# Kernel optimization log

Hardware: AMD Instinct MI355X
Metric: run time of the kernel (lower is better)

Reference implementation:

```python
import jax, jax.numpy as jnp
import numpy as np

B, T, D, E, C = 4, 4096, 2048, 8, 1024
H = D // E  # per-expert hidden = out_features // num_experts = 256


def setup_inputs() -> dict:
    key = jax.random.key(0)
    ks = jax.random.split(key, 7)
    x = jax.random.normal(ks[0], (B, T, D), dtype=jnp.float32)
    # nn.Linear-style init scale ~ 1/sqrt(fan_in)
    W1 = jax.random.normal(ks[1], (E, H, D), dtype=jnp.float32) / np.sqrt(D)
    b1 = jax.random.normal(ks[2], (E, H), dtype=jnp.float32) / np.sqrt(D)
    W2 = jax.random.normal(ks[3], (E, D, H), dtype=jnp.float32) / np.sqrt(D)
    b2 = jax.random.normal(ks[4], (D,), dtype=jnp.float32) / np.sqrt(D)
    expert_indices = jax.random.randint(ks[5], (B, E, C), 0, T, dtype=jnp.int32)
    expert_gate = jax.random.uniform(ks[6], (B, E, C), dtype=jnp.float32)
    return {"x": x, "W1": W1, "b1": b1, "W2": W2, "b2": b2,
            "expert_indices": expert_indices, "expert_gate": expert_gate,
            "num_tokens": T}


def reference(x, W1, b1, W2, b2, expert_indices, expert_gate, num_tokens):
    # x: (B,T,D); expert_indices/expert_gate: (B,E,C)
    Bb = x.shape[0]
    Ee, Cc = expert_indices.shape[1], expert_indices.shape[2]
    b_idx = jnp.arange(Bb)[:, None, None]
    # dispatch: gather tokens per expert -> (B,E,C,D)
    sel = x[b_idx, expert_indices]
    # contract: per-expert GEMM -> (B,E,C,H)
    h = jnp.einsum('becd,ehd->bech', sel, W1) + b1[None, :, None, :]
    h = jax.nn.gelu(h, approximate=False)
    # expand: per-expert GEMM -> (B,E,C,D), shared output bias
    y = jnp.einsum('bech,eoh->beco', h, W2) + b2
    y = y * expert_gate[..., None]
    # combine: gated scatter-add back to token positions -> (B,T,D)
    out = jnp.zeros((Bb, num_tokens, x.shape[2]), dtype=x.dtype)
    out = out.at[jnp.arange(Bb)[:, None], expert_indices.reshape(Bb, Ee * Cc)].add(
        y.reshape(Bb, Ee * Cc, -1))
    return out
```

## Files before the change

kernel.cpp:

```cpp
#include <hip/hip_runtime.h>
#include <math.h>

#define B_ 4
#define T_ 4096
#define D_ 2048
#define E_ 8
#define C_ 1024
#define H_ 256
#define SLOTCAP 32

typedef unsigned short u16;
typedef unsigned long long u64;
typedef __attribute__((ext_vector_type(8))) short short8;
typedef __attribute__((ext_vector_type(4))) float f32x4;

__device__ __forceinline__ u16 f2bf(float f) {
    union { float f; unsigned u; } v; v.f = f;
    unsigned r = (v.u + 0x7FFFu + ((v.u >> 16) & 1u)) >> 16;
    return (u16)r;
}
__device__ __forceinline__ float bf2f(u16 u) {
    union { unsigned u; float f; } v; v.u = ((unsigned)u) << 16;
    return v.f;
}

__device__ __forceinline__ int swz(int row, int chunk) {
    return (row << 6) + ((chunk ^ (row & 7)) << 3);
}

__global__ __launch_bounds__(256) void conv_f32_bf16(
    const float* __restrict__ src, u16* __restrict__ dst, int n)
{
    int i = (blockIdx.x * 256 + threadIdx.x) * 4;
    if (i >= n) return;
    f32x4 v = *reinterpret_cast<const f32x4*>(src + i);
    u16 o[4];
    o[0] = f2bf(v[0]); o[1] = f2bf(v[1]); o[2] = f2bf(v[2]); o[3] = f2bf(v[3]);
    *reinterpret_cast<u64*>(dst + i) = *reinterpret_cast<const u64*>(o);
}

__global__ __launch_bounds__(512) void gemm1_v3(
    const float* __restrict__ x, const u16* __restrict__ W1bf,
    const float* __restrict__ b1, const int* __restrict__ idx,
    u16* __restrict__ Hbuf)
{
    const int mt = blockIdx.x;
    const int be = blockIdx.y;
    const int b = be >> 3, e = be & 7;
    const int m0 = mt * 128;

    __shared__ __align__(16) u16 As[2][128 * 64];
    __shared__ __align__(16) u16 Bs[2][256 * 64];
    __shared__ int toks[128];
    __shared__ float bs1[256];

    const int tid = threadIdx.x;
    if (tid < 128) toks[tid] = idx[(b * E_ + e) * C_ + m0 + tid];
    if (tid < 256) bs1[tid] = b1[e * H_ + tid];
    __syncthreads();

    const int lane = tid & 63, wid = tid >> 6;
    const int wm = wid >> 2, wn = wid & 3;
    const int l15 = lane & 15, lk = lane >> 4;

    const int ar = tid >> 2, ac0 = tid & 3;
    const float* aRow = x + (size_t)b * (T_ * (size_t)D_)
                          + (size_t)toks[ar] * D_;
    const int br = tid >> 1, bc0 = (tid & 1) * 4;
    const u16* bRow = W1bf + ((size_t)e * H_ + br) * D_;

    const int aOff0 = swz(ar, ac0), aOff1 = swz(ar, ac0 + 4);
    int bOff[4];
    #pragma unroll
    for (int j = 0; j < 4; ++j) bOff[j] = swz(br, bc0 + j);

    f32x4 acc[4][4];
    #pragma unroll
    for (int i = 0; i < 4; ++i)
        #pragma unroll
        for (int j = 0; j < 4; ++j)
            acc[i][j] = (f32x4){0.f, 0.f, 0.f, 0.f};

    f32x4 pa[4];
    short8 pb[4];

#define G1_LOAD(k)                                                            \
    do {                                                                      \
        pa[0] = *reinterpret_cast<const f32x4*>(aRow + (k) + ac0 * 8);        \
        pa[1] = *reinterpret_cast<const f32x4*>(aRow + (k) + ac0 * 8 + 4);    \
        pa[2] = *reinterpret_cast<const f32x4*>(aRow + (k) + (ac0 + 4) * 8);  \
        pa[3] = *reinterpret_cast<const f32x4*>(aRow + (k) + (ac0 + 4) * 8 + 4);\
        _Pragma("unroll")                                                     \
        for (int j = 0; j < 4; ++j)                                           \
            pb[j] = *reinterpret_cast<const short8*>(bRow + (k) + (bc0 + j) * 8);\
    } while (0)

#define G1_WRITE(buf)                                                         \
    do {                                                                      \
        short8 s0, s1;                                                        \
        _Pragma("unroll")                                                     \
        for (int r = 0; r < 4; ++r) {                                         \
            s0[r] = (short)f2bf(pa[0][r]); s0[r + 4] = (short)f2bf(pa[1][r]); \
            s1[r] = (short)f2bf(pa[2][r]); s1[r + 4] = (short)f2bf(pa[3][r]); \
        }                                                                     \
        *reinterpret_cast<short8*>(&As[buf][aOff0]) = s0;                     \
        *reinterpret_cast<short8*>(&As[buf][aOff1]) = s1;                     \
        _Pragma("unroll")                                                     \
        for (int j = 0; j < 4; ++j)                                           \
            *reinterpret_cast<short8*>(&Bs[buf][bOff[j]]) = pb[j];            \
    } while (0)

    G1_LOAD(0);
    G1_WRITE(0);
    G1_LOAD(64);
    asm volatile("s_waitcnt lgkmcnt(0)" ::: "memory");
    __builtin_amdgcn_s_barrier();

    const int NT = D_ / 64;
    for (int t = 0; t < NT; ++t) {
        const int cur = t & 1;
        if (t + 1 < NT) G1_WRITE(cur ^ 1);
        if (t + 2 < NT) G1_LOAD((t + 2) * 64);
        #pragma unroll
        for (int kk = 0; kk < 2; ++kk) {
            short8 af[4], bfr[4];
            #pragma unroll
            for (int m = 0; m < 4; ++m) {
                const int row = wm * 64 + m * 16 + l15;
                af[m] = *reinterpret_cast<const short8*>(
                    &As[cur][swz(row, kk * 4 + lk)]);
            }
            #pragma unroll
            for (int n = 0; n < 4; ++n) {
                const int row = wn * 64 + n * 16 + l15;
                bfr[n] = *reinterpret_cast<const short8*>(
                    &Bs[cur][swz(row, kk * 4 + lk)]);
            }
            #pragma unroll
            for (int m = 0; m < 4; ++m)
                #pragma unroll
                for (int n = 0; n < 4; ++n)
                    acc[m][n] = __builtin_amdgcn_mfma_f32_16x16x32_bf16(
                        bfr[n], af[m], acc[m][n], 0, 0, 0);
        }
        asm volatile("s_waitcnt lgkmcnt(0)" ::: "memory");
        __builtin_amdgcn_s_barrier();
    }
#undef G1_LOAD
#undef G1_WRITE

    const size_t hbase = ((size_t)(b * E_ + e) * C_ + m0) * H_;
    #pragma unroll
    for (int m = 0; m < 4; ++m) {
        const int cl = wm * 64 + m * 16 + l15;
        u16* rowp = Hbuf + hbase + (size_t)cl * H_;
        #pragma unroll
        for (int n = 0; n < 4; ++n) {
            const int hb = wn * 64 + n * 16 + lk * 4;
            u16 o[4];
            #pragma unroll
            for (int r = 0; r < 4; ++r) {
                float h = acc[m][n][r] + bs1[hb + r];
                float g = 0.5f * h * (1.0f + erff(h * 0.70710678118f));
                o[r] = f2bf(g);
            }
            *reinterpret_cast<u64*>(rowp + hb) = *reinterpret_cast<const u64*>(o);
        }
    }
}

__global__ __launch_bounds__(512) void gemm2_v2(
    const u16* __restrict__ Hbuf, const u16* __restrict__ W2bf,
    const float* __restrict__ b2, const float* __restrict__ gate,
    u16* __restrict__ Ybuf)
{
    const int mt = blockIdx.x >> 3, nt = blockIdx.x & 7;
    const int be = blockIdx.y;
    const int b = be >> 3, e = be & 7;
    const int m0 = mt * 128, n0 = nt * 256;

    __shared__ __align__(16) u16 As[128 * 64];
    __shared__ __align__(16) u16 Bs[256 * 64];
    __shared__ float gs[128];
    __shared__ float bs2[256];

    const int tid = threadIdx.x;
    if (tid < 128) gs[tid] = gate[(b * E_ + e) * C_ + m0 + tid];
    if (tid < 256) bs2[tid] = b2[n0 + tid];
    __syncthreads();

    const int lane = tid & 63, wid = tid >> 6;
    const int wm = wid >> 2, wn = wid & 3;
    const int l15 = lane & 15, lk = lane >> 4;

    const int ar = tid >> 2, ac0 = tid & 3;
    const u16* aRow = Hbuf + ((size_t)(b * E_ + e) * C_ + m0 + ar) * H_;
    const int br = tid >> 1, bc0 = (tid & 1) * 4;
    const u16* bRow = W2bf + ((size_t)e * D_ + n0 + br) * H_;

    const int aOff0 = swz(ar, ac0), aOff1 = swz(ar, ac0 + 4);
    int bOff[4];
    #pragma unroll
    for (int j = 0; j < 4; ++j) bOff[j] = swz(br, bc0 + j);

    f32x4 acc[4][4];
    #pragma unroll
    for (int i = 0; i < 4; ++i)
        #pragma unroll
        for (int j = 0; j < 4; ++j)
            acc[i][j] = (f32x4){0.f, 0.f, 0.f, 0.f};

    short8 pa0, pa1, pb[4];
    pa0 = *reinterpret_cast<const short8*>(aRow + ac0 * 8);
    pa1 = *reinterpret_cast<const short8*>(aRow + (ac0 + 4) * 8);
    #pragma unroll
    for (int j = 0; j < 4; ++j)
        pb[j] = *reinterpret_cast<const short8*>(bRow + (bc0 + j) * 8);
    *reinterpret_cast<short8*>(&As[aOff0]) = pa0;
    *reinterpret_cast<short8*>(&As[aOff1]) = pa1;
    #pragma unroll
    for (int j = 0; j < 4; ++j)
        *reinterpret_cast<short8*>(&Bs[bOff[j]]) = pb[j];
    __syncthreads();

    const int NT = H_ / 64;
    for (int t = 0; t < NT; ++t) {
        if (t + 1 < NT) {
            const int k = (t + 1) * 64;
            pa0 = *reinterpret_cast<const short8*>(aRow + k + ac0 * 8);
            pa1 = *reinterpret_cast<const short8*>(aRow + k + (ac0 + 4) * 8);
            #pragma unroll
            for (int j = 0; j < 4; ++j)
                pb[j] = *reinterpret_cast<const short8*>(bRow + k + (bc0 + j) * 8);
        }
        #pragma unroll
        for (int kk = 0; kk < 2; ++kk) {
            short8 af[4], bfr[4];
            #pragma unroll
            for (int m = 0; m < 4; ++m) {
                const int row = wm * 64 + m * 16 + l15;
                af[m] = *reinterpret_cast<const short8*>(&As[swz(row, kk * 4 + lk)]);
            }
            #pragma unroll
            for (int n = 0; n < 4; ++n) {
                const int row = wn * 64 + n * 16 + l15;
                bfr[n] = *reinterpret_cast<const short8*>(&Bs[swz(row, kk * 4 + lk)]);
            }
            #pragma unroll
            for (int m = 0; m < 4; ++m)
                #pragma unroll
                for (int n = 0; n < 4; ++n)
                    acc[m][n] = __builtin_amdgcn_mfma_f32_16x16x32_bf16(
                        bfr[n], af[m], acc[m][n], 0, 0, 0);
        }
        if (t + 1 < NT) {
            __syncthreads();
            *reinterpret_cast<short8*>(&As[aOff0]) = pa0;
            *reinterpret_cast<short8*>(&As[aOff1]) = pa1;
            #pragma unroll
            for (int j = 0; j < 4; ++j)
                *reinterpret_cast<short8*>(&Bs[bOff[j]]) = pb[j];
            __syncthreads();
        }
    }

    const size_t ybase = (size_t)(b * E_ + e) * C_ + m0;
    #pragma unroll
    for (int m = 0; m < 4; ++m) {
        const int cl = wm * 64 + m * 16 + l15;
        const float g = gs[cl];
        u16* rowp = Ybuf + (ybase + cl) * (size_t)D_ + n0;
        #pragma unroll
        for (int n = 0; n < 4; ++n) {
            const int db = wn * 64 + n * 16 + lk * 4;
            u16 o[4];
            #pragma unroll
            for (int r = 0; r < 4; ++r)
                o[r] = f2bf((acc[m][n][r] + bs2[db + r]) * g);
            *reinterpret_cast<u64*>(rowp + db) = *reinterpret_cast<const u64*>(o);
        }
    }
}

__global__ __launch_bounds__(256) void fill_kernel(
    const int* __restrict__ idx, int* __restrict__ cnt,
    int* __restrict__ slots)
{
    int i = blockIdx.x * 256 + threadIdx.x;
    if (i >= B_ * E_ * C_) return;
    int b = i / (E_ * C_);
    int slot = i % (E_ * C_);
    int t = idx[i];
    int p = atomicAdd(&cnt[b * T_ + t], 1);
    if (p < SLOTCAP) slots[(b * T_ + t) * SLOTCAP + p] = slot;
}

__global__ __launch_bounds__(256) void combine_kernel(
    const u16* __restrict__ Ybuf, const int* __restrict__ cnt,
    const int* __restrict__ slots, float* __restrict__ out)
{
    const int bt = blockIdx.x;
    const int tid = threadIdx.x;
    __shared__ int sl[SLOTCAP];
    int n = cnt[bt];
    n = n > SLOTCAP ? SLOTCAP : n;
    if (tid < n) sl[tid] = slots[bt * SLOTCAP + tid];
    __syncthreads();
    const int b = bt >> 12;
    float a[8] = {0.f, 0.f, 0.f, 0.f, 0.f, 0.f, 0.f, 0.f};
    for (int s = 0; s < n; ++s) {
        const u16* yrow = Ybuf + ((size_t)b * (E_ * C_) + sl[s]) * D_ + tid * 8;
        short8 v = *reinterpret_cast<const short8*>(yrow);
        #pragma unroll
        for (int j = 0; j < 8; ++j) a[j] += bf2f((u16)v[j]);
    }
    float* orow = out + (size_t)bt * D_ + tid * 8;
    *reinterpret_cast<f32x4*>(orow)     = (f32x4){a[0], a[1], a[2], a[3]};
    *reinterpret_cast<f32x4*>(orow + 4) = (f32x4){a[4], a[5], a[6], a[7]};
}

extern "C" void kernel_launch(void* const* d_in, const int* in_sizes, int n_in,
                              void* d_out, int out_size, void* d_ws, size_t ws_size,
                              hipStream_t stream) {
    const float* x    = (const float*)d_in[0];
    const float* W1   = (const float*)d_in[1];
    const float* b1   = (const float*)d_in[2];
    const float* W2   = (const float*)d_in[3];
    const float* b2   = (const float*)d_in[4];
    const int*   idx  = (const int*)d_in[5];
    const float* gate = (const float*)d_in[6];
    float* out = (float*)d_out;

    const size_t nW = (size_t)E_ * H_ * D_;
    const size_t nH = (size_t)B_ * E_ * C_ * H_;
    const size_t nY = (size_t)B_ * E_ * C_ * D_;

    u16* W1bf = (u16*)d_ws;
    u16* W2bf = W1bf + nW;
    u16* Hbuf = W2bf + nW;
    u16* Ybuf = Hbuf + nH;
    int* cnt   = (int*)(Ybuf + nY);
    int* slots = cnt + (size_t)B_ * T_;

    hipMemsetAsync(cnt, 0, (size_t)B_ * T_ * sizeof(int), stream);
    conv_f32_bf16<<<(int)(nW / 1024), 256, 0, stream>>>(W1, W1bf, (int)nW);
    conv_f32_bf16<<<(int)(nW / 1024), 256, 0, stream>>>(W2, W2bf, (int)nW);
    fill_kernel<<<(B_ * E_ * C_) / 256, 256, 0, stream>>>(idx, cnt, slots);

    gemm1_v3<<<dim3(8, 32), 512, 0, stream>>>(x, W1bf, b1, idx, Hbuf);
    gemm2_v2<<<dim3(64, 32), 512, 0, stream>>>(Hbuf, W2bf, b2, gate, Ybuf);
    combine_kernel<<<B_ * T_, 256, 0, stream>>>(Ybuf, cnt, slots, out);
}
```

Measured before the change: 219.0 us.

## Split gemm1 into 128x128 tiles with 256-thread blocks and MFMA priority

gemm1 now splits the 256-wide hidden dimension into two 128-column tiles and uses 256-thread blocks with two blocks per CU. This doubles the grid to 512 blocks, which should fill the CUs better and reduce LDS per block. It also raises wave priority around the MFMA loop and switches to the library bf16 conversion. The cost is that each gathered x row is now loaded and converted twice, once per N tile.

```diff
diff --git a/kernel.cpp b/kernel.cpp
--- a/kernel.cpp
+++ b/kernel.cpp
@@ -1,4 +1,5 @@
 #include <hip/hip_runtime.h>
+#include <hip/hip_bf16.h>
 #include <math.h>
 
 #define B_ 4
@@ -19,6 +20,11 @@
     unsigned r = (v.u + 0x7FFFu + ((v.u >> 16) & 1u)) >> 16;
     return (u16)r;
 }
+__device__ __forceinline__ u16 f2bf_n(float f) {
+    union { __hip_bfloat16 b; u16 u; } v;
+    v.b = __float2bfloat16(f);
+    return v.u;
+}
 __device__ __forceinline__ float bf2f(u16 u) {
     union { unsigned u; float f; } v; v.u = ((unsigned)u) << 16;
     return v.f;
@@ -39,40 +45,42 @@
     *reinterpret_cast<u64*>(dst + i) = *reinterpret_cast<const u64*>(o);
 }
 
-__global__ __launch_bounds__(512) void gemm1_v3(
+__global__ __launch_bounds__(256, 2) void gemm1_v4(
     const float* __restrict__ x, const u16* __restrict__ W1bf,
     const float* __restrict__ b1, const int* __restrict__ idx,
     u16* __restrict__ Hbuf)
 {
-    const int mt = blockIdx.x;
+    const int mt = blockIdx.x >> 1, nt = blockIdx.x & 1;
     const int be = blockIdx.y;
     const int b = be >> 3, e = be & 7;
-    const int m0 = mt * 128;
+    const int m0 = mt * 128, n0 = nt * 128;
 
     __shared__ __align__(16) u16 As[2][128 * 64];
-    __shared__ __align__(16) u16 Bs[2][256 * 64];
+    __shared__ __align__(16) u16 Bs[2][128 * 64];
     __shared__ int toks[128];
-    __shared__ float bs1[256];
+    __shared__ float bs1[128];
 
     const int tid = threadIdx.x;
-    if (tid < 128) toks[tid] = idx[(b * E_ + e) * C_ + m0 + tid];
-    if (tid < 256) bs1[tid] = b1[e * H_ + tid];
+    if (tid < 128) {
+        toks[tid] = idx[(b * E_ + e) * C_ + m0 + tid];
+        bs1[tid] = b1[e * H_ + n0 + tid];
+    }
     __syncthreads();
 
     const int lane = tid & 63, wid = tid >> 6;
-    const int wm = wid >> 2, wn = wid & 3;
+    const int wm = wid >> 1, wn = wid & 1;
     const int l15 = lane & 15, lk = lane >> 4;
 
-    const int ar = tid >> 2, ac0 = tid & 3;
+    const int sr = tid >> 1;
+    const int scb = (tid & 1) * 4;
+
     const float* aRow = x + (size_t)b * (T_ * (size_t)D_)
-                          + (size_t)toks[ar] * D_;
-    const int br = tid >> 1, bc0 = (tid & 1) * 4;
-    const u16* bRow = W1bf + ((size_t)e * H_ + br) * D_;
-
-    const int aOff0 = swz(ar, ac0), aOff1 = swz(ar, ac0 + 4);
-    int bOff[4];
-    #pragma unroll
-    for (int j = 0; j < 4; ++j) bOff[j] = swz(br, bc0 + j);
+                          + (size_t)toks[sr] * D_;
+    const u16* bRow = W1bf + ((size_t)e * H_ + n0 + sr) * D_;
+
+    int wOff[4];
+    #pragma unroll
+    for (int j = 0; j < 4; ++j) wOff[j] = swz(sr, scb + j);
 
     f32x4 acc[4][4];
     #pragma unroll
@@ -81,33 +89,32 @@
         for (int j = 0; j < 4; ++j)
             acc[i][j] = (f32x4){0.f, 0.f, 0.f, 0.f};
 
-    f32x4 pa[4];
+    f32x4 pa[8];
     short8 pb[4];
 
-#define G1_LOAD(k)                                                            \
-    do {                                                                      \
-        pa[0] = *reinterpret_cast<const f32x4*>(aRow + (k) + ac0 * 8);        \
-        pa[1] = *reinterpret_cast<const f32x4*>(aRow + (k) + ac0 * 8 + 4);    \
-        pa[2] = *reinterpret_cast<const f32x4*>(aRow + (k) + (ac0 + 4) * 8);  \
-        pa[3] = *reinterpret_cast<const f32x4*>(aRow + (k) + (ac0 + 4) * 8 + 4);\
-        _Pragma("unroll")                                                     \
-        for (int j = 0; j < 4; ++j)                                           \
-            pb[j] = *reinterpret_cast<const short8*>(bRow + (k) + (bc0 + j) * 8);\
+#define G1_LOAD(k)                                                             \
+    do {                                                                       \
+        _Pragma("unroll")                                                      \
+        for (int j = 0; j < 4; ++j) {                                          \
+            pa[2 * j]     = *reinterpret_cast<const f32x4*>(aRow + (k) + (scb + j) * 8);     \
+            pa[2 * j + 1] = *reinterpret_cast<const f32x4*>(aRow + (k) + (scb + j) * 8 + 4); \
+            pb[j] = *reinterpret_cast<const short8*>(bRow + (k) + (scb + j) * 8);            \
+        }                                                                      \
     } while (0)
 
-#define G1_WRITE(buf)                                                         \
-    do {                                                                      \
-        short8 s0, s1;                                                        \
-        _Pragma("unroll")                                                     \
-        for (int r = 0; r < 4; ++r) {                                         \
-            s0[r] = (short)f2bf(pa[0][r]); s0[r + 4] = (short)f2bf(pa[1][r]); \
-            s1[r] = (short)f2bf(pa[2][r]); s1[r + 4] = (short)f2bf(pa[3][r]); \
-        }                                                                     \
-        *reinterpret_cast<short8*>(&As[buf][aOff0]) = s0;                     \
-        *reinterpret_cast<short8*>(&As[buf][aOff1]) = s1;                     \
-        _Pragma("unroll")                                                     \
-        for (int j = 0; j < 4; ++j)                                           \
-            *reinterpret_cast<short8*>(&Bs[buf][bOff[j]]) = pb[j];            \
+#define G1_WRITE(buf)                                                          \
+    do {                                                                       \
+        _Pragma("unroll")                                                      \
+        for (int j = 0; j < 4; ++j) {                                          \
+            short8 s;                                                          \
+            _Pragma("unroll")                                                  \
+            for (int r = 0; r < 4; ++r) {                                      \
+                s[r]     = (short)f2bf_n(pa[2 * j][r]);                        \
+                s[r + 4] = (short)f2bf_n(pa[2 * j + 1][r]);                    \
+            }                                                                  \
+            *reinterpret_cast<short8*>(&As[buf][wOff[j]]) = s;                 \
+            *reinterpret_cast<short8*>(&Bs[buf][wOff[j]]) = pb[j];             \
+        }                                                                      \
     } while (0)
 
     G1_LOAD(0);
@@ -136,12 +143,14 @@
                 bfr[n] = *reinterpret_cast<const short8*>(
                     &Bs[cur][swz(row, kk * 4 + lk)]);
             }
+            __builtin_amdgcn_s_setprio(1);
             #pragma unroll
             for (int m = 0; m < 4; ++m)
                 #pragma unroll
                 for (int n = 0; n < 4; ++n)
                     acc[m][n] = __builtin_amdgcn_mfma_f32_16x16x32_bf16(
                         bfr[n], af[m], acc[m][n], 0, 0, 0);
+            __builtin_amdgcn_s_setprio(0);
         }
         asm volatile("s_waitcnt lgkmcnt(0)" ::: "memory");
         __builtin_amdgcn_s_barrier();
@@ -153,7 +162,7 @@
     #pragma unroll
     for (int m = 0; m < 4; ++m) {
         const int cl = wm * 64 + m * 16 + l15;
-        u16* rowp = Hbuf + hbase + (size_t)cl * H_;
+        u16* rowp = Hbuf + hbase + (size_t)cl * H_ + n0;
         #pragma unroll
         for (int n = 0; n < 4; ++n) {
             const int hb = wn * 64 + n * 16 + lk * 4;
@@ -162,7 +171,7 @@
             for (int r = 0; r < 4; ++r) {
                 float h = acc[m][n][r] + bs1[hb + r];
                 float g = 0.5f * h * (1.0f + erff(h * 0.70710678118f));
-                o[r] = f2bf(g);
+                o[r] = f2bf_n(g);
             }
             *reinterpret_cast<u64*>(rowp + hb) = *reinterpret_cast<const u64*>(o);
         }
@@ -347,7 +356,7 @@
     conv_f32_bf16<<<(int)(nW / 1024), 256, 0, stream>>>(W2, W2bf, (int)nW);
     fill_kernel<<<(B_ * E_ * C_) / 256, 256, 0, stream>>>(idx, cnt, slots);
 
-    gemm1_v3<<<dim3(8, 32), 512, 0, stream>>>(x, W1bf, b1, idx, Hbuf);
+    gemm1_v4<<<dim3(16, 32), 256, 0, stream>>>(x, W1bf, b1, idx, Hbuf);
     gemm2_v2<<<dim3(64, 32), 512, 0, stream>>>(Hbuf, W2bf, b2, gate, Ybuf);
     combine_kernel<<<B_ * T_, 256, 0, stream>>>(Ybuf, cnt, slots, out);
 }
```

Measured after the change: 264.1 us. 1.21x slower.

## Double-buffer gemm2 LDS tiles, raise MFMA priority, use native bf16 conversion

Applied to the files above, without the earlier changes.

gemm2 switches from a single LDS buffer guarded by two barriers per K-step to a double-buffered scheme with a register prefetch two tiles ahead and one barrier per step, matching gemm1. Both GEMMs wrap their MFMA blocks in s_setprio(1)/s_setprio(0) so the matrix-core work is favoured over other waves. The manual round-to-nearest bf16 conversion is replaced with the HIP intrinsic __float2bfloat16. Double-buffering doubles gemm2's LDS footprint, and with only 4 K-steps in gemm2 the pipelining gain may be small.

```diff
diff --git a/kernel.cpp b/kernel.cpp
--- a/kernel.cpp
+++ b/kernel.cpp
@@ -1,4 +1,5 @@
 #include <hip/hip_runtime.h>
+#include <hip/hip_bf16.h>
 #include <math.h>
 
 #define B_ 4
@@ -19,6 +20,11 @@
     unsigned r = (v.u + 0x7FFFu + ((v.u >> 16) & 1u)) >> 16;
     return (u16)r;
 }
+__device__ __forceinline__ u16 f2bf_n(float f) {
+    union { __hip_bfloat16 b; u16 u; } v;
+    v.b = __float2bfloat16(f);
+    return v.u;
+}
 __device__ __forceinline__ float bf2f(u16 u) {
     union { unsigned u; float f; } v; v.u = ((unsigned)u) << 16;
     return v.f;
@@ -39,7 +45,7 @@
     *reinterpret_cast<u64*>(dst + i) = *reinterpret_cast<const u64*>(o);
 }
 
-__global__ __launch_bounds__(512) void gemm1_v3(
+__global__ __launch_bounds__(512) void gemm1_v5(
     const float* __restrict__ x, const u16* __restrict__ W1bf,
     const float* __restrict__ b1, const int* __restrict__ idx,
     u16* __restrict__ Hbuf)
@@ -100,8 +106,8 @@
         short8 s0, s1;                                                        \
         _Pragma("unroll")                                                     \
         for (int r = 0; r < 4; ++r) {                                         \
-            s0[r] = (short)f2bf(pa[0][r]); s0[r + 4] = (short)f2bf(pa[1][r]); \
-            s1[r] = (short)f2bf(pa[2][r]); s1[r + 4] = (short)f2bf(pa[3][r]); \
+            s0[r] = (short)f2bf_n(pa[0][r]); s0[r + 4] = (short)f2bf_n(pa[1][r]); \
+            s1[r] = (short)f2bf_n(pa[2][r]); s1[r + 4] = (short)f2bf_n(pa[3][r]); \
         }                                                                     \
         *reinterpret_cast<short8*>(&As[buf][aOff0]) = s0;                     \
         *reinterpret_cast<short8*>(&As[buf][aOff1]) = s1;                     \
@@ -136,12 +142,14 @@
                 bfr[n] = *reinterpret_cast<const short8*>(
                     &Bs[cur][swz(row, kk * 4 + lk)]);
             }
+            __builtin_amdgcn_s_setprio(1);
             #pragma unroll
             for (int m = 0; m < 4; ++m)
                 #pragma unroll
                 for (int n = 0; n < 4; ++n)
                     acc[m][n] = __builtin_amdgcn_mfma_f32_16x16x32_bf16(
                         bfr[n], af[m], acc[m][n], 0, 0, 0);
+            __builtin_amdgcn_s_setprio(0);
         }
         asm volatile("s_waitcnt lgkmcnt(0)" ::: "memory");
         __builtin_amdgcn_s_barrier();
@@ -162,14 +170,14 @@
             for (int r = 0; r < 4; ++r) {
                 float h = acc[m][n][r] + bs1[hb + r];
                 float g = 0.5f * h * (1.0f + erff(h * 0.70710678118f));
-                o[r] = f2bf(g);
+                o[r] = f2bf_n(g);
             }
             *reinterpret_cast<u64*>(rowp + hb) = *reinterpret_cast<const u64*>(o);
         }
     }
 }
 
-__global__ __launch_bounds__(512) void gemm2_v2(
+__global__ __launch_bounds__(512) void gemm2_v3(
     const u16* __restrict__ Hbuf, const u16* __restrict__ W2bf,
     const float* __restrict__ b2, const float* __restrict__ gate,
     u16* __restrict__ Ybuf)
@@ -179,8 +187,8 @@
     const int b = be >> 3, e = be & 7;
     const int m0 = mt * 128, n0 = nt * 256;
 
-    __shared__ __align__(16) u16 As[128 * 64];
-    __shared__ __align__(16) u16 Bs[256 * 64];
+    __shared__ __align__(16) u16 As[2][128 * 64];
+    __shared__ __align__(16) u16 Bs[2][256 * 64];
     __shared__ float gs[128];
     __shared__ float bs2[256];
 
@@ -211,58 +219,65 @@
             acc[i][j] = (f32x4){0.f, 0.f, 0.f, 0.f};
 
     short8 pa0, pa1, pb[4];
-    pa0 = *reinterpret_cast<const short8*>(aRow + ac0 * 8);
-    pa1 = *reinterpret_cast<const short8*>(aRow + (ac0 + 4) * 8);
-    #pragma unroll
-    for (int j = 0; j < 4; ++j)
-        pb[j] = *reinterpret_cast<const short8*>(bRow + (bc0 + j) * 8);
-    *reinterpret_cast<short8*>(&As[aOff0]) = pa0;
-    *reinterpret_cast<short8*>(&As[aOff1]) = pa1;
-    #pragma unroll
-    for (int j = 0; j < 4; ++j)
-        *reinterpret_cast<short8*>(&Bs[bOff[j]]) = pb[j];
-    __syncthreads();
+
+#define G2_LOAD(k)                                                            \
+    do {                                                                      \
+        pa0 = *reinterpret_cast<const short8*>(aRow + (k) + ac0 * 8);         \
+        pa1 = *reinterpret_cast<const short8*>(aRow + (k) + (ac0 + 4) * 8);   \
+        _Pragma("unroll")                                                     \
+        for (int j = 0; j < 4; ++j)                                           \
+            pb[j] = *reinterpret_cast<const short8*>(bRow + (k) + (bc0 + j) * 8);\
+    } while (0)
+
+#define G2_WRITE(buf)                                                         \
+    do {                                                                      \
+        *reinterpret_cast<short8*>(&As[buf][aOff0]) = pa0;                    \
+        *reinterpret_cast<short8*>(&As[buf][aOff1]) = pa1;                    \
+        _Pragma("unroll")                                                     \
+        for (int j = 0; j < 4; ++j)                                           \
+            *reinterpret_cast<short8*>(&Bs[buf][bOff[j]]) = pb[j];            \
+    } while (0)
+
+    G2_LOAD(0);
+    G2_WRITE(0);
+    G2_LOAD(64);
+    asm volatile("s_waitcnt lgkmcnt(0)" ::: "memory");
+    __builtin_amdgcn_s_barrier();
 
     const int NT = H_ / 64;
     for (int t = 0; t < NT; ++t) {
-        if (t + 1 < NT) {
-            const int k = (t + 1) * 64;
-            pa0 = *reinterpret_cast<const short8*>(aRow + k + ac0 * 8);
-            pa1 = *reinterpret_cast<const short8*>(aRow + k + (ac0 + 4) * 8);
-            #pragma unroll
-            for (int j = 0; j < 4; ++j)
-                pb[j] = *reinterpret_cast<const short8*>(bRow + k + (bc0 + j) * 8);
-        }
+        const int cur = t & 1;
+        if (t + 1 < NT) G2_WRITE(cur ^ 1);
+        if (t + 2 < NT) G2_LOAD((t + 2) * 64);
         #pragma unroll
         for (int kk = 0; kk < 2; ++kk) {
             short8 af[4], bfr[4];
             #pragma unroll
             for (int m = 0; m < 4; ++m) {
                 const int row = wm * 64 + m * 16 + l15;
-                af[m] = *reinterpret_cast<const short8*>(&As[swz(row, kk * 4 + lk)]);
+                af[m] = *reinterpret_cast<const short8*>(
+                    &As[cur][swz(row, kk * 4 + lk)]);
             }
             #pragma unroll
             for (int n = 0; n < 4; ++n) {
                 const int row = wn * 64 + n * 16 + l15;
-                bfr[n] = *reinterpret_cast<const short8*>(&Bs[swz(row, kk * 4 + lk)]);
-            }
+                bfr[n] = *reinterpret_cast<const short8*>(
+                    &Bs[cur][swz(row, kk * 4 + lk)]);
+            }
+            __builtin_amdgcn_s_setprio(1);
             #pragma unroll
             for (int m = 0; m < 4; ++m)
                 #pragma unroll
                 for (int n = 0; n < 4; ++n)
                     acc[m][n] = __builtin_amdgcn_mfma_f32_16x16x32_bf16(
                         bfr[n], af[m], acc[m][n], 0, 0, 0);
+            __builtin_amdgcn_s_setprio(0);
         }
-        if (t + 1 < NT) {
-            __syncthreads();
-            *reinterpret_cast<short8*>(&As[aOff0]) = pa0;
-            *reinterpret_cast<short8*>(&As[aOff1]) = pa1;
-            #pragma unroll
-            for (int j = 0; j < 4; ++j)
-                *reinterpret_cast<short8*>(&Bs[bOff[j]]) = pb[j];
-            __syncthreads();
-        }
-    }
+        asm volatile("s_waitcnt lgkmcnt(0)" ::: "memory");
+        __builtin_amdgcn_s_barrier();
+    }
+#undef G2_LOAD
+#undef G2_WRITE
 
     const size_t ybase = (size_t)(b * E_ + e) * C_ + m0;
     #pragma unroll
@@ -276,7 +291,7 @@
             u16 o[4];
             #pragma unroll
             for (int r = 0; r < 4; ++r)
-                o[r] = f2bf((acc[m][n][r] + bs2[db + r]) * g);
+                o[r] = f2bf_n((acc[m][n][r] + bs2[db + r]) * g);
             *reinterpret_cast<u64*>(rowp + db) = *reinterpret_cast<const u64*>(o);
         }
     }
@@ -347,7 +362,7 @@
     conv_f32_bf16<<<(int)(nW / 1024), 256, 0, stream>>>(W2, W2bf, (int)nW);
     fill_kernel<<<(B_ * E_ * C_) / 256, 256, 0, stream>>>(idx, cnt, slots);
 
-    gemm1_v3<<<dim3(8, 32), 512, 0, stream>>>(x, W1bf, b1, idx, Hbuf);
-    gemm2_v2<<<dim3(64, 32), 512, 0, stream>>>(Hbuf, W2bf, b2, gate, Ybuf);
+    gemm1_v5<<<dim3(8, 32), 512, 0, stream>>>(x, W1bf, b1, idx, Hbuf);
+    gemm2_v3<<<dim3(64, 32), 512, 0, stream>>>(Hbuf, W2bf, b2, gate, Ybuf);
     combine_kernel<<<B_ * T_, 256, 0, stream>>>(Ybuf, cnt, slots, out);
 }
```

New measurement: 231.1 us. 1.06x slower.
